# Performance work log

Hardware: AMD Instinct MI355X
Metric: run time of the kernel (lower is better)

The kernel has to match this reference:

```python
import jax, jax.numpy as jnp
import numpy as np

N, E = 50000, 800000
DIM_IN, DIM_H, DIM_OUT, HEADS = 128, 16, 64, 8
NEG_SLOPE = 0.2  # PyG GATv2Conv default


def setup_inputs() -> dict:
    key = jax.random.key(0)
    ks = jax.random.split(key, 10)
    s = 0.1
    x = jax.random.normal(ks[0], (N, DIM_IN), jnp.float32)
    edge_index = jax.random.randint(ks[1], (2, E), 0, N, dtype=jnp.int32)
    Wl1 = jax.random.normal(ks[2], (DIM_IN, HEADS * DIM_H), jnp.float32) * s
    Wr1 = jax.random.normal(ks[3], (DIM_IN, HEADS * DIM_H), jnp.float32) * s
    att1 = jax.random.normal(ks[4], (HEADS, DIM_H), jnp.float32) * s
    b1 = jnp.zeros((HEADS * DIM_H,), jnp.float32)
    Wl2 = jax.random.normal(ks[5], (HEADS * DIM_H, DIM_OUT), jnp.float32) * s
    Wr2 = jax.random.normal(ks[6], (HEADS * DIM_H, DIM_OUT), jnp.float32) * s
    att2 = jax.random.normal(ks[7], (1, DIM_OUT), jnp.float32) * s
    b2 = jnp.zeros((DIM_OUT,), jnp.float32)
    return dict(x=x, edge_index=edge_index, Wl1=Wl1, Wr1=Wr1, att1=att1, b1=b1,
                Wl2=Wl2, Wr2=Wr2, att2=att2, b2=b2)


def gatv2_conv(x, src, dst, Wl, Wr, att, bias, heads, out_ch):
    # PyG GATv2Conv (share_weights=False, concat=True)
    n = x.shape[0]
    xl = (x @ Wl).reshape(n, heads, out_ch)  # source-side transform
    xr = (x @ Wr).reshape(n, heads, out_ch)  # target-side transform
    e = jax.nn.leaky_relu(xl[src] + xr[dst], NEG_SLOPE)          # [E, H, C]
    logits = jnp.einsum('ehc,hc->eh', e, att)                    # [E, H]
    # segment softmax over incoming edges of each dst node
    m = jax.lax.stop_gradient(jax.ops.segment_max(logits, dst, num_segments=n))
    ex = jnp.exp(logits - m[dst])
    denom = jax.ops.segment_sum(ex, dst, num_segments=n)
    alpha = ex / denom[dst]                                      # [E, H]
    out = jax.ops.segment_sum(xl[src] * alpha[..., None], dst, num_segments=n)
    return out.reshape(n, heads * out_ch) + bias


def reference(x, edge_index, Wl1, Wr1, att1, b1, Wl2, Wr2, att2, b2):
    n = x.shape[0]
    loops = jnp.arange(n, dtype=edge_index.dtype)
    src = jnp.concatenate([edge_index[0], loops])  # add_self_loops=True
    dst = jnp.concatenate([edge_index[1], loops])
    h = gatv2_conv(x, src, dst, Wl1, Wr1, att1, b1, HEADS, DIM_H)
    h = jax.nn.elu(h)
    out = gatv2_conv(h, src, dst, Wl2, Wr2, att2, b2, 1, DIM_OUT)
    return jax.nn.log_softmax(out, axis=1)
```

## Files before the change

kernel.cpp:

```cpp
#include <hip/hip_runtime.h>
#include <cstdint>

#define DIM_IN 128
#define HEADS 8
#define DIM_H 16
#define H1 128
#define DIM_OUT 64
#define NEG 0.2f
#define CAP 6144

typedef __attribute__((ext_vector_type(8))) short bf16x8;
typedef __attribute__((ext_vector_type(4))) float f32x4;

__device__ __forceinline__ float blo(uint32_t u) { return __uint_as_float(u << 16); }
__device__ __forceinline__ float bhi(uint32_t u) { return __uint_as_float(u & 0xffff0000u); }
__device__ __forceinline__ unsigned short f2b(float f) {
  uint32_t u = __float_as_uint(f);
  u += 0x7fffu + ((u >> 16) & 1u);
  return (unsigned short)(u >> 16);
}

__global__ __launch_bounds__(256) void conv_x(
    const float* __restrict__ in, unsigned short* __restrict__ out, int total) {
  int i = (blockIdx.x * 256 + threadIdx.x) * 8;
  if (i >= total) return;
  float4 a = *(const float4*)(in + i);
  float4 b = *(const float4*)(in + i + 4);
  ushort4 u0 = {f2b(a.x), f2b(a.y), f2b(a.z), f2b(a.w)};
  ushort4 u1 = {f2b(b.x), f2b(b.y), f2b(b.z), f2b(b.w)};
  *(ushort4*)(out + i) = u0;
  *(ushort4*)(out + i + 4) = u1;
}

__global__ __launch_bounds__(256) void prep_w(
    const float* __restrict__ W0, const float* __restrict__ W1,
    const float* __restrict__ W2, const float* __restrict__ W3,
    unsigned short* __restrict__ T0, unsigned short* __restrict__ T1,
    unsigned short* __restrict__ T2, unsigned short* __restrict__ T3) {
  int z = blockIdx.y;
  const float* W = (z == 0) ? W0 : (z == 1) ? W1 : (z == 2) ? W2 : W3;
  unsigned short* T = (z == 0) ? T0 : (z == 1) ? T1 : (z == 2) ? T2 : T3;
  int M = (z < 2) ? 128 : 64;
  int t = blockIdx.x * 256 + threadIdx.x;
  if (t >= M * 128) return;
  int n = t >> 7, k = t & 127;
  T[t] = f2b(W[k * M + n]);
}

template <int M>
__global__ __launch_bounds__(256) void gemm_mfma(
    const unsigned short* __restrict__ A,
    const unsigned short* __restrict__ Bt0, const unsigned short* __restrict__ Bt1,
    unsigned short* __restrict__ Cb0, float* __restrict__ C1, int Nrows) {
  constexpr int K = 128;
  constexpr int LDA = 72;
  constexpr int MT = M / 2;
  constexpr int NT = MT / 16;
  __shared__ __align__(16) short Asm[128 * LDA];
  __shared__ __align__(16) short Bsm[M * LDA];
  const unsigned short* __restrict__ Bt = blockIdx.z ? Bt1 : Bt0;
  const int row0 = blockIdx.x * 128;
  const int tid = threadIdx.x;
  const int w = tid >> 6, lane = tid & 63;
  const int l = lane & 15, q = lane >> 4;
  const int wrow = (w >> 1) * 64, wcol = (w & 1) * MT;

  f32x4 zero = {0.f, 0.f, 0.f, 0.f};
  f32x4 acc[4][NT];
#pragma unroll
  for (int ti = 0; ti < 4; ++ti)
#pragma unroll
    for (int tj = 0; tj < NT; ++tj) acc[ti][tj] = zero;

  for (int k0 = 0; k0 < K; k0 += 64) {
    __syncthreads();
    {
      int r = tid >> 1, sg = (tid & 1) * 32;
      int grow = row0 + r;
      const uint4* src = (const uint4*)(A + (size_t)grow * K + k0 + sg);
      uint4 z4 = make_uint4(0, 0, 0, 0);
#pragma unroll
      for (int i = 0; i < 4; ++i) {
        uint4 v = (grow < Nrows) ? src[i] : z4;
        *(uint4*)(Asm + r * LDA + sg + i * 8) = v;
      }
    }
    {
      int r = tid >> 1, sg = (tid & 1) * 32;
      if (r < M) {
        const uint4* src = (const uint4*)(Bt + (size_t)r * K + k0 + sg);
#pragma unroll
        for (int i = 0; i < 4; ++i)
          *(uint4*)(Bsm + r * LDA + sg + i * 8) = src[i];
      }
    }
    __syncthreads();
#pragma unroll
    for (int kk = 0; kk < 64; kk += 32) {
      bf16x8 af[4], bfr[NT];
#pragma unroll
      for (int ti = 0; ti < 4; ++ti)
        af[ti] = *(const bf16x8*)(Asm + (wrow + ti * 16 + l) * LDA + kk + q * 8);
#pragma unroll
      for (int tj = 0; tj < NT; ++tj)
        bfr[tj] = *(const bf16x8*)(Bsm + (wcol + tj * 16 + l) * LDA + kk + q * 8);
#pragma unroll
      for (int ti = 0; ti < 4; ++ti)
#pragma unroll
        for (int tj = 0; tj < NT; ++tj)
          acc[ti][tj] = __builtin_amdgcn_mfma_f32_16x16x32_bf16(
              af[ti], bfr[tj], acc[ti][tj], 0, 0, 0);
    }
  }
#pragma unroll
  for (int ti = 0; ti < 4; ++ti) {
#pragma unroll
    for (int tj = 0; tj < NT; ++tj) {
      int col = wcol + tj * 16 + l;
#pragma unroll
      for (int r = 0; r < 4; ++r) {
        int grow = row0 + wrow + ti * 16 + q * 4 + r;
        if (grow < Nrows) {
          float vv = acc[ti][tj][r];
          if (blockIdx.z == 0) Cb0[(size_t)grow * M + col] = f2b(vv);
          else                 C1[(size_t)grow * M + col] = vv;
        }
      }
    }
  }
}


__global__ __launch_bounds__(256) void p1_bucket(
    const int* __restrict__ ei, int* __restrict__ gcnt,
    uint32_t* __restrict__ gbuf, int E, int nbkt) {
  __shared__ int hist[256];
  __shared__ int base[256];
  __shared__ int cur[256];
  int tid = threadIdx.x;
  hist[tid] = 0;
  __syncthreads();
  int e0 = blockIdx.x * 8192;
  int nE = min(8192, E - e0);
  for (int i = tid; i < nE; i += 256)
    atomicAdd(&hist[ei[E + e0 + i] >> 8], 1);
  __syncthreads();
  if (tid < nbkt) {
    int h = hist[tid];
    base[tid] = h ? atomicAdd(&gcnt[tid], h) : 0;
  }
  cur[tid] = 0;
  __syncthreads();
  for (int i = tid; i < nE; i += 256) {
    int d = ei[E + e0 + i];
    int s = ei[e0 + i];
    int b = d >> 8;
    int r = atomicAdd(&cur[b], 1);
    int pos = base[b] + r;
    if (pos < CAP) gbuf[(size_t)b * CAP + pos] = ((uint32_t)d << 16) | (uint32_t)s;
  }
}

__global__ __launch_bounds__(256) void p2a_hist(
    const uint32_t* __restrict__ gbuf, const int* __restrict__ gcnt,
    int* __restrict__ deg, int N) {
  __shared__ int hist[256];
  int b = blockIdx.x, tid = threadIdx.x;
  hist[tid] = 0;
  __syncthreads();
  int cnt = min(gcnt[b], CAP);
  const uint32_t* p = gbuf + (size_t)b * CAP;
  for (int i = tid; i < cnt; i += 256)
    atomicAdd(&hist[(p[i] >> 16) & 255], 1);
  __syncthreads();
  int node = (b << 8) + tid;
  if (node < N) deg[node] = hist[tid];
}

__global__ __launch_bounds__(256) void p2b_scatter(
    const uint32_t* __restrict__ gbuf, const int* __restrict__ gcnt,
    const int* __restrict__ off, int* __restrict__ srcs, int N) {
  __shared__ int cur[256];
  int b = blockIdx.x, tid = threadIdx.x;
  int node = (b << 8) + tid;
  cur[tid] = (node < N) ? off[node] : 0;
  __syncthreads();
  int cnt = min(gcnt[b], CAP);
  const uint32_t* p = gbuf + (size_t)b * CAP;
  for (int i = tid; i < cnt; i += 256) {
    uint32_t v = p[i];
    int pos = atomicAdd(&cur[(v >> 16) & 255], 1);
    srcs[pos] = (int)(v & 0xFFFFu);
  }
}

__global__ __launch_bounds__(256) void scan_part(
    const int* __restrict__ deg, int* __restrict__ bsum, int N) {
  int i = blockIdx.x * 256 + threadIdx.x;
  int v = (i < N) ? deg[i] : 0;
#pragma unroll
  for (int o = 1; o < 64; o <<= 1) v += __shfl_xor(v, o, 64);
  __shared__ int wsums[4];
  if ((threadIdx.x & 63) == 0) wsums[threadIdx.x >> 6] = v;
  __syncthreads();
  if (threadIdx.x == 0)
    bsum[blockIdx.x] = wsums[0] + wsums[1] + wsums[2] + wsums[3];
}

__global__ __launch_bounds__(256) void scan_tops(
    int* __restrict__ bsum, int* __restrict__ offN, int nb) {
  int tid = threadIdx.x;
  int lane = tid & 63, wid = tid >> 6;
  int v = (tid < nb) ? bsum[tid] : 0;
  int x = v;
#pragma unroll
  for (int o = 1; o < 64; o <<= 1) {
    int y = __shfl_up(x, o, 64);
    if (lane >= o) x += y;
  }
  __shared__ int ws[4];
  if (lane == 63) ws[wid] = x;
  __syncthreads();
  int prefix = 0;
  for (int w = 0; w < 4; ++w) if (w < wid) prefix += ws[w];
  int incl = prefix + x;
  if (tid < nb) bsum[tid] = incl - v;
  if (tid == 255) *offN = incl;
}

__global__ __launch_bounds__(256) void scan_final(
    const int* __restrict__ deg, const int* __restrict__ bsum,
    int* __restrict__ off, int N) {
  int i = blockIdx.x * 256 + threadIdx.x;
  int lane = threadIdx.x & 63, wid = threadIdx.x >> 6;
  int v = (i < N) ? deg[i] : 0;
  int x = v;
#pragma unroll
  for (int o = 1; o < 64; o <<= 1) {
    int y = __shfl_up(x, o, 64);
    if (lane >= o) x += y;
  }
  __shared__ int ws[4];
  if (lane == 63) ws[wid] = x;
  __syncthreads();
  int prefix = bsum[blockIdx.x];
  for (int w = 0; w < 4; ++w) if (w < wid) prefix += ws[w];
  int excl = prefix + x - v;
  if (i < N) off[i] = excl;
}

__global__ __launch_bounds__(256) void agg_l1(
    const int* __restrict__ srcs, const int* __restrict__ off,
    const unsigned short* __restrict__ xlb, const float* __restrict__ xr,
    const float* __restrict__ att, const float* __restrict__ b1,
    unsigned short* __restrict__ hbb, int N) {
  int wid = threadIdx.x >> 6, lane = threadIdx.x & 63;
  int node = blockIdx.x * 4 + wid;
  if (node >= N) return;
  const int l4 = lane & 15;
  const int g  = lane >> 4;
  float4 xr0 = *(const float4*)(xr + ((size_t)node << 7) + (l4 << 3));
  float4 xr1 = *(const float4*)(xr + ((size_t)node << 7) + (l4 << 3) + 4);
  float4 a0  = *(const float4*)(att + (l4 << 3));
  float4 a1  = *(const float4*)(att + (l4 << 3) + 4);
  float acc0 = 0.f, acc1 = 0.f, acc2 = 0.f, acc3 = 0.f;
  float acc4 = 0.f, acc5 = 0.f, acc6 = 0.f, acc7 = 0.f;
  float dsum = 0.f;
  int beg = off[node];
  int M = off[node + 1] - beg + 1;
  for (int base = 0; base < M; base += 64) {
    int nk = min(64, M - base);
    int v = base + lane;
    int sv = 0;
    if (lane < nk) sv = (v == 0) ? node : srcs[beg + v - 1];
    int niter = (nk + 3) >> 2;
    for (int it = 0; it < niter; ++it) {
      int j = (it << 2) + g;
      int s = __shfl(sv, j, 64);
      uint4 xu = *(const uint4*)(xlb + ((size_t)s << 7) + (l4 << 3));
      float x0 = blo(xu.x), x1 = bhi(xu.x), x2 = blo(xu.y), x3 = bhi(xu.y);
      float x4 = blo(xu.z), x5 = bhi(xu.z), x6 = blo(xu.w), x7 = bhi(xu.w);
      float t, p;
      t = x0 + xr0.x; t = t > 0.f ? t : NEG * t; p = a0.x * t;
      t = x1 + xr0.y; t = t > 0.f ? t : NEG * t; p = fmaf(a0.y, t, p);
      t = x2 + xr0.z; t = t > 0.f ? t : NEG * t; p = fmaf(a0.z, t, p);
      t = x3 + xr0.w; t = t > 0.f ? t : NEG * t; p = fmaf(a0.w, t, p);
      t = x4 + xr1.x; t = t > 0.f ? t : NEG * t; p = fmaf(a1.x, t, p);
      t = x5 + xr1.y; t = t > 0.f ? t : NEG * t; p = fmaf(a1.y, t, p);
      t = x6 + xr1.z; t = t > 0.f ? t : NEG * t; p = fmaf(a1.z, t, p);
      t = x7 + xr1.w; t = t > 0.f ? t : NEG * t; p = fmaf(a1.w, t, p);
      p += __shfl_xor(p, 1, 64);
      float ev = (j < nk) ? __expf(p) : 0.f;
      acc0 = fmaf(ev, x0, acc0); acc1 = fmaf(ev, x1, acc1);
      acc2 = fmaf(ev, x2, acc2); acc3 = fmaf(ev, x3, acc3);
      acc4 = fmaf(ev, x4, acc4); acc5 = fmaf(ev, x5, acc5);
      acc6 = fmaf(ev, x6, acc6); acc7 = fmaf(ev, x7, acc7);
      dsum += ev;
    }
  }
#pragma unroll
  for (int o = 16; o <= 32; o <<= 1) {
    dsum += __shfl_xor(dsum, o, 64);
    acc0 += __shfl_xor(acc0, o, 64); acc1 += __shfl_xor(acc1, o, 64);
    acc2 += __shfl_xor(acc2, o, 64); acc3 += __shfl_xor(acc3, o, 64);
    acc4 += __shfl_xor(acc4, o, 64); acc5 += __shfl_xor(acc5, o, 64);
    acc6 += __shfl_xor(acc6, o, 64); acc7 += __shfl_xor(acc7, o, 64);
  }
  if (g == 0) {
    float inv = 1.0f / dsum;
    float4 bv0 = *(const float4*)(b1 + (l4 << 3));
    float4 bv1 = *(const float4*)(b1 + (l4 << 3) + 4);
    float o0 = fmaf(acc0, inv, bv0.x), o1 = fmaf(acc1, inv, bv0.y);
    float o2 = fmaf(acc2, inv, bv0.z), o3 = fmaf(acc3, inv, bv0.w);
    float o4 = fmaf(acc4, inv, bv1.x), o5 = fmaf(acc5, inv, bv1.y);
    float o6 = fmaf(acc6, inv, bv1.z), o7 = fmaf(acc7, inv, bv1.w);
    o0 = o0 > 0.f ? o0 : expm1f(o0); o1 = o1 > 0.f ? o1 : expm1f(o1);
    o2 = o2 > 0.f ? o2 : expm1f(o2); o3 = o3 > 0.f ? o3 : expm1f(o3);
    o4 = o4 > 0.f ? o4 : expm1f(o4); o5 = o5 > 0.f ? o5 : expm1f(o5);
    o6 = o6 > 0.f ? o6 : expm1f(o6); o7 = o7 > 0.f ? o7 : expm1f(o7);
    ushort4 h0 = {f2b(o0), f2b(o1), f2b(o2), f2b(o3)};
    ushort4 h1 = {f2b(o4), f2b(o5), f2b(o6), f2b(o7)};
    unsigned short* ph = hbb + ((size_t)node << 7) + (l4 << 3);
    *(ushort4*)(ph)     = h0;
    *(ushort4*)(ph + 4) = h1;
  }
}

__global__ __launch_bounds__(256) void agg_l2(
    const int* __restrict__ srcs, const int* __restrict__ off,
    const unsigned short* __restrict__ xlb, const float* __restrict__ xr,
    const float* __restrict__ att, const float* __restrict__ b2,
    float* __restrict__ out, int N) {
  int wid = threadIdx.x >> 6, lane = threadIdx.x & 63;
  int node = blockIdx.x * 4 + wid;
  if (node >= N) return;
  const int l3 = lane & 7;
  const int g  = lane >> 3;
  float4 xr0 = *(const float4*)(xr + ((size_t)node << 6) + (l3 << 3));
  float4 xr1 = *(const float4*)(xr + ((size_t)node << 6) + (l3 << 3) + 4);
  float4 a0  = *(const float4*)(att + (l3 << 3));
  float4 a1  = *(const float4*)(att + (l3 << 3) + 4);
  float acc0 = 0.f, acc1 = 0.f, acc2 = 0.f, acc3 = 0.f;
  float acc4 = 0.f, acc5 = 0.f, acc6 = 0.f, acc7 = 0.f;
  float dsum = 0.f;
  int beg = off[node];
  int M = off[node + 1] - beg + 1;
  for (int base = 0; base < M; base += 64) {
    int nk = min(64, M - base);
    int v = base + lane;
    int sv = 0;
    if (lane < nk) sv = (v == 0) ? node : srcs[beg + v - 1];
    int niter = (nk + 7) >> 3;
    for (int it = 0; it < niter; ++it) {
      int j = (it << 3) + g;
      int s = __shfl(sv, j, 64);
      uint4 xu = *(const uint4*)(xlb + ((size_t)s << 6) + (l3 << 3));
      float x0 = blo(xu.x), x1 = bhi(xu.x), x2 = blo(xu.y), x3 = bhi(xu.y);
      float x4 = blo(xu.z), x5 = bhi(xu.z), x6 = blo(xu.w), x7 = bhi(xu.w);
      float t, p;
      t = x0 + xr0.x; t = t > 0.f ? t : NEG * t; p = a0.x * t;
      t = x1 + xr0.y; t = t > 0.f ? t : NEG * t; p = fmaf(a0.y, t, p);
      t = x2 + xr0.z; t = t > 0.f ? t : NEG * t; p = fmaf(a0.z, t, p);
      t = x3 + xr0.w; t = t > 0.f ? t : NEG * t; p = fmaf(a0.w, t, p);
      t = x4 + xr1.x; t = t > 0.f ? t : NEG * t; p = fmaf(a1.x, t, p);
      t = x5 + xr1.y; t = t > 0.f ? t : NEG * t; p = fmaf(a1.y, t, p);
      t = x6 + xr1.z; t = t > 0.f ? t : NEG * t; p = fmaf(a1.z, t, p);
      t = x7 + xr1.w; t = t > 0.f ? t : NEG * t; p = fmaf(a1.w, t, p);
      p += __shfl_xor(p, 1, 64);
      p += __shfl_xor(p, 2, 64);
      p += __shfl_xor(p, 4, 64);
      float ev = (j < nk) ? __expf(p) : 0.f;
      acc0 = fmaf(ev, x0, acc0); acc1 = fmaf(ev, x1, acc1);
      acc2 = fmaf(ev, x2, acc2); acc3 = fmaf(ev, x3, acc3);
      acc4 = fmaf(ev, x4, acc4); acc5 = fmaf(ev, x5, acc5);
      acc6 = fmaf(ev, x6, acc6); acc7 = fmaf(ev, x7, acc7);
      dsum += ev;
    }
  }
#pragma unroll
  for (int o = 8; o <= 32; o <<= 1) {
    dsum += __shfl_xor(dsum, o, 64);
    acc0 += __shfl_xor(acc0, o, 64); acc1 += __shfl_xor(acc1, o, 64);
    acc2 += __shfl_xor(acc2, o, 64); acc3 += __shfl_xor(acc3, o, 64);
    acc4 += __shfl_xor(acc4, o, 64); acc5 += __shfl_xor(acc5, o, 64);
    acc6 += __shfl_xor(acc6, o, 64); acc7 += __shfl_xor(acc7, o, 64);
  }
  float inv = 1.0f / dsum;
  float4 bv0 = *(const float4*)(b2 + (l3 << 3));
  float4 bv1 = *(const float4*)(b2 + (l3 << 3) + 4);
  float v0 = fmaf(acc0, inv, bv0.x), v1 = fmaf(acc1, inv, bv0.y);
  float v2 = fmaf(acc2, inv, bv0.z), v3 = fmaf(acc3, inv, bv0.w);
  float v4 = fmaf(acc4, inv, bv1.x), v5 = fmaf(acc5, inv, bv1.y);
  float v6 = fmaf(acc6, inv, bv1.z), v7 = fmaf(acc7, inv, bv1.w);
  float m = fmaxf(fmaxf(fmaxf(v0, v1), fmaxf(v2, v3)),
                  fmaxf(fmaxf(v4, v5), fmaxf(v6, v7)));
#pragma unroll
  for (int o = 1; o <= 4; o <<= 1) m = fmaxf(m, __shfl_xor(m, o, 64));
  float s = __expf(v0 - m) + __expf(v1 - m) + __expf(v2 - m) + __expf(v3 - m)
          + __expf(v4 - m) + __expf(v5 - m) + __expf(v6 - m) + __expf(v7 - m);
#pragma unroll
  for (int o = 1; o <= 4; o <<= 1) s += __shfl_xor(s, o, 64);
  if (g == 0) {
    float ls = __logf(s) + m;
    float* po = out + ((size_t)node << 6) + (l3 << 3);
    *(float4*)(po)     = make_float4(v0 - ls, v1 - ls, v2 - ls, v3 - ls);
    *(float4*)(po + 4) = make_float4(v4 - ls, v5 - ls, v6 - ls, v7 - ls);
  }
}

extern "C" void kernel_launch(void* const* d_in, const int* in_sizes, int n_in,
                              void* d_out, int out_size, void* d_ws, size_t ws_size,
                              hipStream_t stream) {
  const float* x    = (const float*)d_in[0];
  const int*   ei   = (const int*)d_in[1];
  const float* Wl1  = (const float*)d_in[2];
  const float* Wr1  = (const float*)d_in[3];
  const float* att1 = (const float*)d_in[4];
  const float* b1   = (const float*)d_in[5];
  const float* Wl2  = (const float*)d_in[6];
  const float* Wr2  = (const float*)d_in[7];
  const float* att2 = (const float*)d_in[8];
  const float* b2   = (const float*)d_in[9];
  float* out = (float*)d_out;

  const int N = in_sizes[0] / DIM_IN;
  const int E = in_sizes[1] / 2;
  const int nb = (N + 255) / 256;

  float* ws = (float*)d_ws;
  const size_t szNH = (size_t)N * H1;
  float* xr1 = ws;
  float* xr2 = ws + szNH;
  unsigned short* xb   = (unsigned short*)(ws + szNH + (size_t)N * DIM_OUT);
  unsigned short* xlb1 = xb + szNH;
  unsigned short* hbb  = xlb1 + szNH;
  unsigned short* xlb2 = hbb + szNH;
  unsigned short* wt0  = xlb2 + (size_t)N * DIM_OUT;
  unsigned short* wt1  = wt0 + 16384;
  unsigned short* wt2  = wt1 + 16384;
  unsigned short* wt3  = wt2 + 8192;
  int* ibase  = (int*)(wt3 + 8192);
  int* deg    = ibase;
  int* off    = ibase + N;
  int* bsum   = ibase + 2 * N + 1;
  int* gcnt   = ibase + 2 * N + 1 + 256;
  int* srcs   = ibase + 2 * N + 1 + 512;
  uint32_t* gbuf = (uint32_t*)(srcs + E);

  hipMemsetAsync(gcnt, 0, 256 * sizeof(int), stream);
  p1_bucket<<<(E + 8191) / 8192, 256, 0, stream>>>(ei, gcnt, gbuf, E, nb);
  p2a_hist<<<nb, 256, 0, stream>>>(gbuf, gcnt, deg, N);
  scan_part<<<nb, 256, 0, stream>>>(deg, bsum, N);
  scan_tops<<<1, 256, 0, stream>>>(bsum, off + N, nb);
  scan_final<<<nb, 256, 0, stream>>>(deg, bsum, off, N);
  p2b_scatter<<<nb, 256, 0, stream>>>(gbuf, gcnt, off, srcs, N);

  int totx = N * DIM_IN;
  conv_x<<<(totx / 8 + 255) / 256, 256, 0, stream>>>(x, xb, totx);
  prep_w<<<dim3(64, 4), 256, 0, stream>>>(Wl1, Wr1, Wl2, Wr2, wt0, wt1, wt2, wt3);

  const int gb = (N + 127) / 128;

  gemm_mfma<128><<<dim3(gb, 1, 2), 256, 0, stream>>>(xb, wt0, wt1, xlb1, xr1, N);
  agg_l1<<<(N + 3) / 4, 256, 0, stream>>>(srcs, off, xlb1, xr1, att1, b1, hbb, N);

  gemm_mfma<64><<<dim3(gb, 1, 2), 256, 0, stream>>>(hbb, wt2, wt3, xlb2, xr2, N);
  agg_l2<<<(N + 3) / 4, 256, 0, stream>>>(srcs, off, xlb2, xr2, att2, b2, out, N);
}
```

Measured before the change: 264.1 us.

## Fuse CSR histogram, prefix scan and scatter into one per-bucket kernel

Replaces the five-kernel CSR build (bucket histogram, three-stage scan, scatter) with one kernel. Each block derives its global base from an exclusive scan of the 256 bucket counts, then computes a local degree histogram, scans it to get node offsets, and scatters sources, all in shared memory. This removes four launches and the round trips of deg/bsum through global memory. Each block redundantly rescans the bucket counts, which is cheap. The edge-bucket data is read twice per block instead of once in each of two kernels.

```diff
diff --git a/kernel.cpp b/kernel.cpp
--- a/kernel.cpp
+++ b/kernel.cpp
@@ -130,7 +130,6 @@
   }
 }
 
-
 __global__ __launch_bounds__(256) void p1_bucket(
     const int* __restrict__ ei, int* __restrict__ gcnt,
     uint32_t* __restrict__ gbuf, int E, int nbkt) {
@@ -161,92 +160,54 @@
   }
 }
 
-__global__ __launch_bounds__(256) void p2a_hist(
+__device__ __forceinline__ int block_excl_scan256(int v, int* tmp) {
+  int lane = threadIdx.x & 63, wid = threadIdx.x >> 6;
+  int x = v;
+#pragma unroll
+  for (int o = 1; o < 64; o <<= 1) {
+    int y = __shfl_up(x, o, 64);
+    if (lane >= o) x += y;
+  }
+  if (lane == 63) tmp[wid] = x;
+  __syncthreads();
+  int prefix = 0;
+#pragma unroll
+  for (int w = 0; w < 4; ++w) if (w < wid) prefix += tmp[w];
+  __syncthreads();
+  return prefix + x - v;
+}
+
+__global__ __launch_bounds__(256) void p2_fused(
     const uint32_t* __restrict__ gbuf, const int* __restrict__ gcnt,
-    int* __restrict__ deg, int N) {
+    int* __restrict__ off, int* __restrict__ srcs, int N, int nbkt) {
+  __shared__ int sb[256];
   __shared__ int hist[256];
+  __shared__ int cur[256];
+  __shared__ int tmp[4];
   int b = blockIdx.x, tid = threadIdx.x;
+  int gv = (tid < nbkt) ? gcnt[tid] : 0;
+  int gex = block_excl_scan256(gv, tmp);
+  sb[tid] = gex;
   hist[tid] = 0;
   __syncthreads();
+  int base = sb[b];
   int cnt = min(gcnt[b], CAP);
   const uint32_t* p = gbuf + (size_t)b * CAP;
   for (int i = tid; i < cnt; i += 256)
     atomicAdd(&hist[(p[i] >> 16) & 255], 1);
   __syncthreads();
-  int node = (b << 8) + tid;
-  if (node < N) deg[node] = hist[tid];
-}
-
-__global__ __launch_bounds__(256) void p2b_scatter(
-    const uint32_t* __restrict__ gbuf, const int* __restrict__ gcnt,
-    const int* __restrict__ off, int* __restrict__ srcs, int N) {
-  __shared__ int cur[256];
-  int b = blockIdx.x, tid = threadIdx.x;
-  int node = (b << 8) + tid;
-  cur[tid] = (node < N) ? off[node] : 0;
-  __syncthreads();
-  int cnt = min(gcnt[b], CAP);
-  const uint32_t* p = gbuf + (size_t)b * CAP;
+  int d = hist[tid];
+  int excl = block_excl_scan256(d, tmp);
+  int idx = (b << 8) + tid;
+  int o = base + excl;
+  if (idx <= N) off[idx] = o;
+  cur[tid] = o;
+  __syncthreads();
   for (int i = tid; i < cnt; i += 256) {
     uint32_t v = p[i];
     int pos = atomicAdd(&cur[(v >> 16) & 255], 1);
     srcs[pos] = (int)(v & 0xFFFFu);
   }
-}
-
-__global__ __launch_bounds__(256) void scan_part(
-    const int* __restrict__ deg, int* __restrict__ bsum, int N) {
-  int i = blockIdx.x * 256 + threadIdx.x;
-  int v = (i < N) ? deg[i] : 0;
-#pragma unroll
-  for (int o = 1; o < 64; o <<= 1) v += __shfl_xor(v, o, 64);
-  __shared__ int wsums[4];
-  if ((threadIdx.x & 63) == 0) wsums[threadIdx.x >> 6] = v;
-  __syncthreads();
-  if (threadIdx.x == 0)
-    bsum[blockIdx.x] = wsums[0] + wsums[1] + wsums[2] + wsums[3];
-}
-
-__global__ __launch_bounds__(256) void scan_tops(
-    int* __restrict__ bsum, int* __restrict__ offN, int nb) {
-  int tid = threadIdx.x;
-  int lane = tid & 63, wid = tid >> 6;
-  int v = (tid < nb) ? bsum[tid] : 0;
-  int x = v;
-#pragma unroll
-  for (int o = 1; o < 64; o <<= 1) {
-    int y = __shfl_up(x, o, 64);
-    if (lane >= o) x += y;
-  }
-  __shared__ int ws[4];
-  if (lane == 63) ws[wid] = x;
-  __syncthreads();
-  int prefix = 0;
-  for (int w = 0; w < 4; ++w) if (w < wid) prefix += ws[w];
-  int incl = prefix + x;
-  if (tid < nb) bsum[tid] = incl - v;
-  if (tid == 255) *offN = incl;
-}
-
-__global__ __launch_bounds__(256) void scan_final(
-    const int* __restrict__ deg, const int* __restrict__ bsum,
-    int* __restrict__ off, int N) {
-  int i = blockIdx.x * 256 + threadIdx.x;
-  int lane = threadIdx.x & 63, wid = threadIdx.x >> 6;
-  int v = (i < N) ? deg[i] : 0;
-  int x = v;
-#pragma unroll
-  for (int o = 1; o < 64; o <<= 1) {
-    int y = __shfl_up(x, o, 64);
-    if (lane >= o) x += y;
-  }
-  __shared__ int ws[4];
-  if (lane == 63) ws[wid] = x;
-  __syncthreads();
-  int prefix = bsum[blockIdx.x];
-  for (int w = 0; w < 4; ++w) if (w < wid) prefix += ws[w];
-  int excl = prefix + x - v;
-  if (i < N) off[i] = excl;
 }
 
 __global__ __launch_bounds__(256) void agg_l1(
@@ -440,20 +401,14 @@
   unsigned short* wt2  = wt1 + 16384;
   unsigned short* wt3  = wt2 + 8192;
   int* ibase  = (int*)(wt3 + 8192);
-  int* deg    = ibase;
-  int* off    = ibase + N;
-  int* bsum   = ibase + 2 * N + 1;
-  int* gcnt   = ibase + 2 * N + 1 + 256;
-  int* srcs   = ibase + 2 * N + 1 + 512;
+  int* off    = ibase;
+  int* gcnt   = ibase + N + 1;
+  int* srcs   = ibase + N + 1 + 256;
   uint32_t* gbuf = (uint32_t*)(srcs + E);
 
   hipMemsetAsync(gcnt, 0, 256 * sizeof(int), stream);
   p1_bucket<<<(E + 8191) / 8192, 256, 0, stream>>>(ei, gcnt, gbuf, E, nb);
-  p2a_hist<<<nb, 256, 0, stream>>>(gbuf, gcnt, deg, N);
-  scan_part<<<nb, 256, 0, stream>>>(deg, bsum, N);
-  scan_tops<<<1, 256, 0, stream>>>(bsum, off + N, nb);
-  scan_final<<<nb, 256, 0, stream>>>(deg, bsum, off, N);
-  p2b_scatter<<<nb, 256, 0, stream>>>(gbuf, gcnt, off, srcs, N);
+  p2_fused<<<nb, 256, 0, stream>>>(gbuf, gcnt, off, srcs, N, nb);
 
   int totx = N * DIM_IN;
   conv_x<<<(totx / 8 + 255) / 256, 256, 0, stream>>>(x, xb, totx);
```

Result: faster. 255.2 us (-3.4%).
